# Kernel optimization log

Hardware: AMD Instinct MI355X
Metric: run time of the kernel (lower is better)

## Reference

```python
import jax, jax.numpy as jnp
import numpy as np

BATCH = 1048576
D_IN = 4        # d_in=3 spatial dims + 1 time dim
HID = 64
N_HID_STACK = 4  # hidden residual blocks after the first hidden layer
D_OUT = 3
BN_EPS = 1e-5


def _bn(x, gamma, beta):
    # BatchNorm1d in training mode: biased batch statistics over the batch axis
    mu = jnp.mean(x, axis=0)
    var = jnp.var(x, axis=0)
    return gamma * (x - mu) * jax.lax.rsqrt(var + BN_EPS) + beta


def setup_inputs() -> dict:
    key = jax.random.key(0)
    ks = jax.random.split(key, 8)
    s_in = 1.0 / np.sqrt(D_IN)
    s_h = 1.0 / np.sqrt(HID)
    return {
        "x": jax.random.normal(ks[0], (BATCH, D_IN), dtype=jnp.float32),
        "bn0_gamma": jnp.ones((D_IN,), jnp.float32),
        "bn0_beta": jnp.zeros((D_IN,), jnp.float32),
        "W0": jax.random.normal(ks[1], (D_IN, HID), jnp.float32) * s_in,
        "b0": jnp.zeros((HID,), jnp.float32),
        "gamma0": jnp.ones((HID,), jnp.float32),
        "beta0": jnp.zeros((HID,), jnp.float32),
        "W_hid": jax.random.normal(ks[2], (N_HID_STACK, HID, HID), jnp.float32) * s_h,
        "b_hid": jnp.zeros((N_HID_STACK, HID), jnp.float32),
        "gamma_hid": jnp.ones((N_HID_STACK, HID), jnp.float32),
        "beta_hid": jnp.zeros((N_HID_STACK, HID), jnp.float32),
        "Wout": jax.random.normal(ks[3], (HID, D_OUT), jnp.float32) * s_h,
        "bout": jnp.zeros((D_OUT,), jnp.float32),
    }


def reference(x, bn0_gamma, bn0_beta, W0, b0, gamma0, beta0,
              W_hid, b_hid, gamma_hid, beta_hid, Wout, bout):
    # Net.forward (u-network, single patch, batch_normalization=True, tanh):
    #   x = bn0(x)
    #   y = bn(act(Linear0(x)))                 (first hidden layer, no skip)
    #   y = bn_i(act(Linear_i(y))) + y          (residual hidden layers)
    #   y = Linear_out(y)
    h = _bn(x, bn0_gamma, bn0_beta)
    y = _bn(jnp.tanh(h @ W0 + b0), gamma0, beta0)

    def step(y, layer):
        W, b, g, be = layer
        return _bn(jnp.tanh(y @ W + b), g, be) + y, None

    y, _ = jax.lax.scan(step, y, (W_hid, b_hid, gamma_hid, beta_hid))
    return y @ Wout + bout
```

## Files before the change

kernel.cpp:

```cpp
#include <hip/hip_runtime.h>
#include <stdint.h>


#define NROWS 1048576
#define EPS 1e-5f
#define INV_B 9.5367431640625e-07f
#define LOG2E2 2.885390081777927f
#define BIGGRID 8192

typedef __attribute__((ext_vector_type(8))) short bfrag;
typedef __attribute__((ext_vector_type(4))) float facc;
typedef __attribute__((ext_vector_type(4))) float f4v;

__device__ __forceinline__ float bf2f(short s) {
  union { unsigned u; float f; } v;
  v.u = ((unsigned)(unsigned short)s) << 16;
  return v.f;
}
__device__ __forceinline__ short f2bf(float f) {
  union { float f; unsigned u; } v;
  v.f = f;
  unsigned r = v.u + 0x7FFFu + ((v.u >> 16) & 1u);
  return (short)(r >> 16);
}
__device__ __forceinline__ float tanh_fast(float x) {
  float e = __builtin_amdgcn_exp2f(x * LOG2E2);
  return 1.f - 2.f * __builtin_amdgcn_rcpf(e + 1.f);
}

__device__ __forceinline__ bfrag make_ident(int l15, int q, int p) {
  bfrag r;
  const short one = (short)0x3F80;
#pragma unroll
  for (int j = 0; j < 8; ++j) r[j] = (q * 8 + j == l15 + 16 * p) ? one : 0;
  return r;
}

template <int W>
__global__ __launch_bounds__(256) void k_reduce(const float* __restrict__ P,
                                                float* __restrict__ S,
                                                int rows_per_blk) {
  __shared__ float red[256];
  const int tid = threadIdx.x;
  const int col = tid % W;
  const int grp = tid / W;
  const int G = 256 / W;
  size_t r0 = (size_t)blockIdx.x * rows_per_blk;
  float s = 0.f;
  for (int r = grp; r < rows_per_blk; r += G) s += P[(r0 + r) * W + col];
  red[tid] = s;
  __syncthreads();
  if (tid < W) {
    float t = 0.f;
#pragma unroll 4
    for (int g = 0; g < G; ++g) t += red[g * W + tid];
    atomicAdd(&S[tid], t);
  }
}


__global__ __launch_bounds__(256) void k_stats_x(const float* __restrict__ x,
                                                 float* __restrict__ P) {
  __shared__ float red[4][8];
  const int tid = threadIdx.x;
  const int wave = tid >> 6;
  size_t base = (size_t)blockIdx.x * 1024 + tid;
  float s[4] = {0.f, 0.f, 0.f, 0.f}, q[4] = {0.f, 0.f, 0.f, 0.f};
#pragma unroll
  for (int it = 0; it < 4; ++it) {
    f4v v = *(const f4v*)(x + (base + (size_t)it * 256) * 4);
#pragma unroll
    for (int k = 0; k < 4; ++k) { s[k] += v[k]; q[k] = fmaf(v[k], v[k], q[k]); }
  }
#pragma unroll
  for (int off = 32; off > 0; off >>= 1) {
#pragma unroll
    for (int k = 0; k < 4; ++k) {
      s[k] += __shfl_xor(s[k], off);
      q[k] += __shfl_xor(q[k], off);
    }
  }
  if ((tid & 63) == 0) {
#pragma unroll
    for (int k = 0; k < 4; ++k) { red[wave][k] = s[k]; red[wave][4 + k] = q[k]; }
  }
  __syncthreads();
  if (tid < 8)
    P[blockIdx.x * 8 + tid] =
        red[0][tid] + red[1][tid] + red[2][tid] + red[3][tid];
}

__global__ __launch_bounds__(256) void k_stats_z1(
    const float* __restrict__ x, const float* __restrict__ bn0g,
    const float* __restrict__ bn0b, const float* __restrict__ W0,
    const float* __restrict__ b0, const float* __restrict__ sx,
    float* __restrict__ P) {
  __shared__ float red[2][4][64];
  const int tid = threadIdx.x;
  const int lane = tid & 63;
  const int wave = tid >> 6;
  int gw = blockIdx.x * 4 + wave;
  float sc[4], sh[4];
#pragma unroll
  for (int k = 0; k < 4; ++k) {
    float mean = sx[k] * INV_B;
    float var = fmaf(-mean, mean, sx[4 + k] * INV_B);
    float rs = rsqrtf(var + EPS);
    sc[k] = bn0g[k] * rs;
    sh[k] = fmaf(-sc[k], mean, bn0b[k]);
  }
  float w[4];
#pragma unroll
  for (int k = 0; k < 4; ++k) w[k] = W0[k * 64 + lane];
  float bj = b0[lane];
  float s = 0.f, q = 0.f;
  size_t r0 = (size_t)gw * 256;
  for (int r = 0; r < 256; ++r) {
    f4v xv = *(const f4v*)(x + (r0 + r) * 4);
    float acc = bj;
#pragma unroll
    for (int k = 0; k < 4; ++k)
      acc = fmaf(fmaf(xv[k], sc[k], sh[k]), w[k], acc);
    float z = tanh_fast(acc);
    s += z;
    q = fmaf(z, z, q);
  }
  red[0][wave][lane] = s;
  red[1][wave][lane] = q;
  __syncthreads();
  if (tid < 128) {
    int which = tid >> 6, c = tid & 63;
    P[blockIdx.x * 128 + tid] = red[which][0][c] + red[which][1][c] +
                                red[which][2][c] + red[which][3][c];
  }
}

__global__ __launch_bounds__(256) void k_prep(const float* __restrict__ Wh,
                                              short* __restrict__ WT) {
  int idx = blockIdx.x * 256 + threadIdx.x;
  int l = idx >> 12, rem = idx & 4095, k = rem >> 6, c = rem & 63;
  WT[l * 4096 + c * 64 + k] = f2bf(Wh[l * 4096 + k * 64 + c]);
}


__global__ __launch_bounds__(256) void k_first(
    const float* __restrict__ x, const float* __restrict__ bn0g,
    const float* __restrict__ bn0b, const float* __restrict__ W0,
    const float* __restrict__ b0, const float* __restrict__ gamma0,
    const float* __restrict__ beta0, const float* __restrict__ sx,
    const float* __restrict__ s1, const short* __restrict__ WTb,
    const float* __restrict__ bb, float* __restrict__ P,
    short* __restrict__ Y) {
  __shared__ __align__(16) float lds_x[128 * 4];
  __shared__ __align__(16) short ly[128 * 72];
  __shared__ float lds_st[4][128];

  const int tid = threadIdx.x;
  const int lane = tid & 63;
  const int wave = tid >> 6;
  const int l15 = lane & 15;
  const int q = lane >> 4;
  const int wr = wave * 32;
  const size_t r0 = (size_t)blockIdx.x * 128;

  f4v xp;
  if (lane < 32) xp = *(const f4v*)(x + (r0 + wr + lane) * 4);

  float sc0[4], sh0[4];
#pragma unroll
  for (int k = 0; k < 4; ++k) {
    float mean = sx[k] * INV_B;
    float var = fmaf(-mean, mean, sx[4 + k] * INV_B);
    float rs = rsqrtf(var + EPS);
    sc0[k] = bn0g[k] * rs;
    sh0[k] = fmaf(-sc0[k], mean, bn0b[k]);
  }
  float w0c[4];
#pragma unroll
  for (int k = 0; k < 4; ++k) w0c[k] = W0[k * 64 + lane];
  float b0c = b0[lane];
  float mean1 = s1[lane] * INV_B;
  float var1 = fmaf(-mean1, mean1, s1[64 + lane] * INV_B);
  float A1c = gamma0[lane] * rsqrtf(var1 + EPS);
  float B1c = fmaf(-A1c, mean1, beta0[lane]);

  if (lane < 32) *(f4v*)&lds_x[(wr + lane) * 4] = xp;

  for (int e = 0; e < 32; ++e) {
    int row = wr + e;
    float acc = b0c;
#pragma unroll
    for (int k = 0; k < 4; ++k)
      acc = fmaf(fmaf(lds_x[row * 4 + k], sc0[k], sh0[k]), w0c[k], acc);
    float z = tanh_fast(acc);
    ly[row * 72 + lane] = f2bf(fmaf(A1c, z, B1c));
  }

  bfrag af[2][2];
#pragma unroll
  for (int mt = 0; mt < 2; ++mt)
#pragma unroll
    for (int kt = 0; kt < 2; ++kt) {
      af[mt][kt] =
          *(const bfrag*)&ly[(wr + mt * 16 + l15) * 72 + kt * 32 + q * 8];
      *(bfrag*)(Y + (r0 + wr + mt * 16 + l15) * 64 + kt * 32 + q * 8) =
          af[mt][kt];
    }
  float bbv[4];
  bfrag bwb[4][2];
#pragma unroll
  for (int nt = 0; nt < 4; ++nt) {
    bbv[nt] = bb[nt * 16 + l15];
#pragma unroll
    for (int kt = 0; kt < 2; ++kt)
      bwb[nt][kt] =
          *(const bfrag*)(WTb + (nt * 16 + l15) * 64 + kt * 32 + q * 8);
  }
  facc acc2[2][4];
#pragma unroll
  for (int mt = 0; mt < 2; ++mt)
#pragma unroll
    for (int nt = 0; nt < 4; ++nt) {
      acc2[mt][nt][0] = bbv[nt]; acc2[mt][nt][1] = bbv[nt];
      acc2[mt][nt][2] = bbv[nt]; acc2[mt][nt][3] = bbv[nt];
    }
#pragma unroll
  for (int mt = 0; mt < 2; ++mt)
#pragma unroll
    for (int nt = 0; nt < 4; ++nt)
#pragma unroll
      for (int kt = 0; kt < 2; ++kt)
        acc2[mt][nt] = __builtin_amdgcn_mfma_f32_16x16x32_bf16(
            af[mt][kt], bwb[nt][kt], acc2[mt][nt], 0, 0, 0);
#pragma unroll
  for (int nt = 0; nt < 4; ++nt) {
    float s = 0.f, ss = 0.f;
#pragma unroll
    for (int mt = 0; mt < 2; ++mt)
#pragma unroll
      for (int i = 0; i < 4; ++i) {
        float z = tanh_fast(acc2[mt][nt][i]);
        s += z;
        ss = fmaf(z, z, ss);
      }
    s += __shfl_xor(s, 16); s += __shfl_xor(s, 32);
    ss += __shfl_xor(ss, 16); ss += __shfl_xor(ss, 32);
    if (q == 0) {
      lds_st[wave][nt * 16 + l15] = s;
      lds_st[wave][64 + nt * 16 + l15] = ss;
    }
  }
  __syncthreads();
  if (tid < 128)
    P[(size_t)blockIdx.x * 128 + tid] =
        lds_st[0][tid] + lds_st[1][tid] + lds_st[2][tid] + lds_st[3][tid];
}

__global__ __launch_bounds__(256) void k_mid(
    short* __restrict__ Y, const short* __restrict__ WTa,
    const float* __restrict__ ba, const float* __restrict__ ga,
    const float* __restrict__ bea, const float* __restrict__ sa,
    const short* __restrict__ WTb, const float* __restrict__ bb,
    float* __restrict__ P, int rev) {
  __shared__ __align__(16) short ly[128 * 72];
  __shared__ float lds_st[4][128];

  const int tid = threadIdx.x;
  const int lane = tid & 63;
  const int wave = tid >> 6;
  const int l15 = lane & 15;
  const int q = lane >> 4;
  const int wr = wave * 32;
  const int bid = rev ? ((int)gridDim.x - 1 - (int)blockIdx.x) : (int)blockIdx.x;
  const size_t r0 = (size_t)bid * 128;

  bfrag af[2][2];
#pragma unroll
  for (int mt = 0; mt < 2; ++mt)
#pragma unroll
    for (int kt = 0; kt < 2; ++kt)
      af[mt][kt] =
          *(const bfrag*)(Y + (r0 + wr + mt * 16 + l15) * 64 + kt * 32 + q * 8);

  float Av[4], Bv[4], bav[4];
#pragma unroll
  for (int nt = 0; nt < 4; ++nt) {
    int c = nt * 16 + l15;
    float mean = sa[c] * INV_B;
    float var = fmaf(-mean, mean, sa[64 + c] * INV_B);
    float A = ga[c] * rsqrtf(var + EPS);
    Av[nt] = A;
    Bv[nt] = fmaf(-A, mean, bea[c]);
    bav[nt] = ba[c];
  }
  bfrag bwa[4][2];
#pragma unroll
  for (int nt = 0; nt < 4; ++nt)
#pragma unroll
    for (int kt = 0; kt < 2; ++kt)
      bwa[nt][kt] =
          *(const bfrag*)(WTa + (nt * 16 + l15) * 64 + kt * 32 + q * 8);
  const bfrag bI0 = make_ident(l15, q, 0);
  const bfrag bI1 = make_ident(l15, q, 1);

#pragma unroll
  for (int mt = 0; mt < 2; ++mt) {
    facc acc[4], yC[4];
#pragma unroll
    for (int nt = 0; nt < 4; ++nt) {
      acc[nt][0] = bav[nt]; acc[nt][1] = bav[nt];
      acc[nt][2] = bav[nt]; acc[nt][3] = bav[nt];
      yC[nt][0] = 0.f; yC[nt][1] = 0.f; yC[nt][2] = 0.f; yC[nt][3] = 0.f;
    }
#pragma unroll
    for (int nt = 0; nt < 4; ++nt) {
#pragma unroll
      for (int kt = 0; kt < 2; ++kt)
        acc[nt] = __builtin_amdgcn_mfma_f32_16x16x32_bf16(
            af[mt][kt], bwa[nt][kt], acc[nt], 0, 0, 0);
      yC[nt] = __builtin_amdgcn_mfma_f32_16x16x32_bf16(
          af[mt][nt >> 1], (nt & 1) ? bI1 : bI0, yC[nt], 0, 0, 0);
    }
#pragma unroll
    for (int nt = 0; nt < 4; ++nt) {
      int c = nt * 16 + l15;
      float A = Av[nt], Bc = Bv[nt];
#pragma unroll
      for (int i = 0; i < 4; ++i) {
        int rl = wr + mt * 16 + q * 4 + i;
        float z = tanh_fast(acc[nt][i]);
        ly[rl * 72 + c] = f2bf(fmaf(A, z, Bc) + yC[nt][i]);
      }
    }
  }

#pragma unroll
  for (int mt = 0; mt < 2; ++mt)
#pragma unroll
    for (int kt = 0; kt < 2; ++kt) {
      af[mt][kt] =
          *(const bfrag*)&ly[(wr + mt * 16 + l15) * 72 + kt * 32 + q * 8];
      *(bfrag*)(Y + (r0 + wr + mt * 16 + l15) * 64 + kt * 32 + q * 8) =
          af[mt][kt];
    }
  float bbv[4];
  bfrag bwb[4][2];
#pragma unroll
  for (int nt = 0; nt < 4; ++nt) {
    bbv[nt] = bb[nt * 16 + l15];
#pragma unroll
    for (int kt = 0; kt < 2; ++kt)
      bwb[nt][kt] =
          *(const bfrag*)(WTb + (nt * 16 + l15) * 64 + kt * 32 + q * 8);
  }
  facc acc2[2][4];
#pragma unroll
  for (int mt = 0; mt < 2; ++mt)
#pragma unroll
    for (int nt = 0; nt < 4; ++nt) {
      acc2[mt][nt][0] = bbv[nt]; acc2[mt][nt][1] = bbv[nt];
      acc2[mt][nt][2] = bbv[nt]; acc2[mt][nt][3] = bbv[nt];
    }
#pragma unroll
  for (int mt = 0; mt < 2; ++mt)
#pragma unroll
    for (int nt = 0; nt < 4; ++nt)
#pragma unroll
      for (int kt = 0; kt < 2; ++kt)
        acc2[mt][nt] = __builtin_amdgcn_mfma_f32_16x16x32_bf16(
            af[mt][kt], bwb[nt][kt], acc2[mt][nt], 0, 0, 0);
#pragma unroll
  for (int nt = 0; nt < 4; ++nt) {
    float s = 0.f, ss = 0.f;
#pragma unroll
    for (int mt = 0; mt < 2; ++mt)
#pragma unroll
      for (int i = 0; i < 4; ++i) {
        float z = tanh_fast(acc2[mt][nt][i]);
        s += z;
        ss = fmaf(z, z, ss);
      }
    s += __shfl_xor(s, 16); s += __shfl_xor(s, 32);
    ss += __shfl_xor(ss, 16); ss += __shfl_xor(ss, 32);
    if (q == 0) {
      lds_st[wave][nt * 16 + l15] = s;
      lds_st[wave][64 + nt * 16 + l15] = ss;
    }
  }
  __syncthreads();
  if (tid < 128)
    P[(size_t)bid * 128 + tid] =
        lds_st[0][tid] + lds_st[1][tid] + lds_st[2][tid] + lds_st[3][tid];
}

__global__ __launch_bounds__(256) void k_last(
    const short* __restrict__ Y, const short* __restrict__ WTa,
    const float* __restrict__ ba, const float* __restrict__ ga,
    const float* __restrict__ bea, const float* __restrict__ sa,
    const float* __restrict__ Wout, const float* __restrict__ bout,
    float* __restrict__ out) {
  const int tid = threadIdx.x;
  const int lane = tid & 63;
  const int wave = tid >> 6;
  const int l15 = lane & 15;
  const int q = lane >> 4;
  const int wr = wave * 32;
  const size_t r0 = (size_t)blockIdx.x * 128;

  bfrag af[2][2];
#pragma unroll
  for (int mt = 0; mt < 2; ++mt)
#pragma unroll
    for (int kt = 0; kt < 2; ++kt)
      af[mt][kt] =
          *(const bfrag*)(Y + (r0 + wr + mt * 16 + l15) * 64 + kt * 32 + q * 8);

  float Av[4], Bv[4], bav[4], wo[4][3];
#pragma unroll
  for (int nt = 0; nt < 4; ++nt) {
    int c = nt * 16 + l15;
    float mean = sa[c] * INV_B;
    float var = fmaf(-mean, mean, sa[64 + c] * INV_B);
    float A = ga[c] * rsqrtf(var + EPS);
    Av[nt] = A;
    Bv[nt] = fmaf(-A, mean, bea[c]);
    bav[nt] = ba[c];
#pragma unroll
    for (int o = 0; o < 3; ++o) wo[nt][o] = Wout[c * 3 + o];
  }
  bfrag bwa[4][2];
#pragma unroll
  for (int nt = 0; nt < 4; ++nt)
#pragma unroll
    for (int kt = 0; kt < 2; ++kt)
      bwa[nt][kt] =
          *(const bfrag*)(WTa + (nt * 16 + l15) * 64 + kt * 32 + q * 8);
  const bfrag bI0 = make_ident(l15, q, 0);
  const bfrag bI1 = make_ident(l15, q, 1);
  float bo0 = bout[0], bo1 = bout[1], bo2 = bout[2];

#pragma unroll
  for (int mt = 0; mt < 2; ++mt) {
    facc acc[4], yC[4];
#pragma unroll
    for (int nt = 0; nt < 4; ++nt) {
      acc[nt][0] = bav[nt]; acc[nt][1] = bav[nt];
      acc[nt][2] = bav[nt]; acc[nt][3] = bav[nt];
      yC[nt][0] = 0.f; yC[nt][1] = 0.f; yC[nt][2] = 0.f; yC[nt][3] = 0.f;
    }
#pragma unroll
    for (int nt = 0; nt < 4; ++nt) {
#pragma unroll
      for (int kt = 0; kt < 2; ++kt)
        acc[nt] = __builtin_amdgcn_mfma_f32_16x16x32_bf16(
            af[mt][kt], bwa[nt][kt], acc[nt], 0, 0, 0);
      yC[nt] = __builtin_amdgcn_mfma_f32_16x16x32_bf16(
          af[mt][nt >> 1], (nt & 1) ? bI1 : bI0, yC[nt], 0, 0, 0);
    }
#pragma unroll
    for (int i = 0; i < 4; ++i) {
      float o0 = 0.f, o1 = 0.f, o2 = 0.f;
#pragma unroll
      for (int nt = 0; nt < 4; ++nt) {
        float z = tanh_fast(acc[nt][i]);
        float yn = bf2f(f2bf(fmaf(Av[nt], z, Bv[nt]) + yC[nt][i]));
        o0 = fmaf(yn, wo[nt][0], o0);
        o1 = fmaf(yn, wo[nt][1], o1);
        o2 = fmaf(yn, wo[nt][2], o2);
      }
#pragma unroll
      for (int off = 1; off < 16; off <<= 1) {
        o0 += __shfl_xor(o0, off);
        o1 += __shfl_xor(o1, off);
        o2 += __shfl_xor(o2, off);
      }
      if (l15 == 0) {
        size_t ro = (r0 + wr + mt * 16 + q * 4 + i) * 3;
        out[ro] = o0 + bo0;
        out[ro + 1] = o1 + bo1;
        out[ro + 2] = o2 + bo2;
      }
    }
  }
}

extern "C" void kernel_launch(void* const* d_in, const int* in_sizes, int n_in,
                              void* d_out, int out_size, void* d_ws,
                              size_t ws_size, hipStream_t stream) {
  (void)in_sizes; (void)n_in; (void)out_size; (void)ws_size;
  const float* x = (const float*)d_in[0];
  const float* bn0g = (const float*)d_in[1];
  const float* bn0b = (const float*)d_in[2];
  const float* W0 = (const float*)d_in[3];
  const float* b0 = (const float*)d_in[4];
  const float* gamma0 = (const float*)d_in[5];
  const float* beta0 = (const float*)d_in[6];
  const float* Wh = (const float*)d_in[7];
  const float* bh = (const float*)d_in[8];
  const float* gh = (const float*)d_in[9];
  const float* beh = (const float*)d_in[10];
  const float* Wout = (const float*)d_in[11];
  const float* bout = (const float*)d_in[12];
  float* out = (float*)d_out;

  char* ws = (char*)d_ws;
  short* Y = (short*)ws;
  const size_t YB = (size_t)NROWS * 64 * 2;
  float* stats = (float*)(ws + YB);
  float* Sx = stats;
  float* S1 = stats + 8;
  float* S2 = stats + 136;
  float* S3 = stats + 264;
  float* S4 = stats + 392;
  float* S5 = stats + 520;
  short* WT = (short*)(ws + YB + 4096);
  float* P = (float*)(ws + YB + 4096 + 32768);

  hipMemsetAsync(stats, 0, 648 * sizeof(float), stream);
  k_prep<<<64, 256, 0, stream>>>(Wh, WT);
  k_stats_x<<<1024, 256, 0, stream>>>(x, P);
  k_reduce<8><<<8, 256, 0, stream>>>(P, Sx, 128);
  k_stats_z1<<<1024, 256, 0, stream>>>(x, bn0g, bn0b, W0, b0, Sx, P);
  k_reduce<128><<<8, 256, 0, stream>>>(P, S1, 128);
  k_first<<<BIGGRID, 256, 0, stream>>>(x, bn0g, bn0b, W0, b0, gamma0, beta0,
                                       Sx, S1, WT, bh, P, Y);
  k_reduce<128><<<64, 256, 0, stream>>>(P, S2, 128);
  k_mid<<<BIGGRID, 256, 0, stream>>>(Y, WT, bh, gh, beh, S2, WT + 4096,
                                     bh + 64, P, 1);
  k_reduce<128><<<64, 256, 0, stream>>>(P, S3, 128);
  k_mid<<<BIGGRID, 256, 0, stream>>>(Y, WT + 4096, bh + 64, gh + 64, beh + 64,
                                     S3, WT + 2 * 4096, bh + 128, P, 0);
  k_reduce<128><<<64, 256, 0, stream>>>(P, S4, 128);
  k_mid<<<BIGGRID, 256, 0, stream>>>(Y, WT + 2 * 4096, bh + 128, gh + 128,
                                     beh + 128, S4, WT + 3 * 4096, bh + 192, P,
                                     1);
  k_reduce<128><<<64, 256, 0, stream>>>(P, S5, 128);
  k_last<<<BIGGRID, 256, 0, stream>>>(Y, WT + 3 * 4096, bh + 192, gh + 192,
                                      beh + 192, S5, Wout, bout, out);
}
```

Baseline: 603.5 us.

## Fuse whole network into one persistent cooperative kernel with grid syncs

Replaces the chain of per-layer kernels and reduce kernels with a single persistent cooperative kernel. Blocks loop over row tiles and exchange BatchNorm statistics through grid.sync-based two-level reductions. This removes roughly a dozen kernel launches and their tail and drain gaps. In exchange it caps occupancy at about two blocks per CU, adds grid-wide barriers, and drops the alternating tile order that used to reuse cache between layers. The old multi-kernel path is kept as a fallback if the cooperative launch fails.

New measurement: 900.1 us. 49.1% more time.

```diff
diff --git a/kernel.cpp b/kernel.cpp
--- a/kernel.cpp
+++ b/kernel.cpp
@@ -1,12 +1,15 @@
 #include <hip/hip_runtime.h>
+#include <hip/hip_cooperative_groups.h>
 #include <stdint.h>
 
+namespace cg = cooperative_groups;
+
 
 #define NROWS 1048576
+#define NTILES 8192
 #define EPS 1e-5f
 #define INV_B 9.5367431640625e-07f
 #define LOG2E2 2.885390081777927f
-#define BIGGRID 8192
 
 typedef __attribute__((ext_vector_type(8))) short bfrag;
 typedef __attribute__((ext_vector_type(4))) float facc;
@@ -27,7 +30,6 @@
   float e = __builtin_amdgcn_exp2f(x * LOG2E2);
   return 1.f - 2.f * __builtin_amdgcn_rcpf(e + 1.f);
 }
-
 __device__ __forceinline__ bfrag make_ident(int l15, int q, int p) {
   bfrag r;
   const short one = (short)0x3F80;
@@ -35,6 +37,433 @@
   for (int j = 0; j < 8; ++j) r[j] = (q * 8 + j == l15 + 16 * p) ? one : 0;
   return r;
 }
+
+
+__device__ __forceinline__ void grid_reduce128(float* __restrict__ P,
+                                               float* __restrict__ P2,
+                                               float* S_lds, float* red_l,
+                                               int bid, int tid, int nblk,
+                                               cg::grid_group& grid) {
+  grid.sync();
+  if (bid < 128 && tid < 128) {
+    float s = 0.f;
+    for (int r = bid; r < nblk; r += 128) s += P[(size_t)r * 128 + tid];
+    P2[bid * 128 + tid] = s;
+  }
+  grid.sync();
+  {
+    int col = tid & 127, g = tid >> 7;
+    float s = 0.f;
+    for (int r = g * 64; r < g * 64 + 64; ++r) s += P2[r * 128 + col];
+    red_l[tid] = s;
+    __syncthreads();
+    if (tid < 128) S_lds[tid] = red_l[tid] + red_l[128 + tid];
+    __syncthreads();
+  }
+}
+
+__global__ __launch_bounds__(256, 2) void k_net(
+    const float* __restrict__ x, const float* __restrict__ bn0g,
+    const float* __restrict__ bn0b, const float* __restrict__ W0,
+    const float* __restrict__ b0, const float* __restrict__ gamma0,
+    const float* __restrict__ beta0, const float* __restrict__ Wh,
+    const float* __restrict__ bh, const float* __restrict__ gh,
+    const float* __restrict__ beh, const float* __restrict__ Wout,
+    const float* __restrict__ bout, short* __restrict__ WT,
+    float* __restrict__ P, float* __restrict__ P2, short* __restrict__ Y,
+    float* __restrict__ out) {
+  cg::grid_group grid = cg::this_grid();
+
+  __shared__ __align__(16) short ly[128 * 72];
+  __shared__ __align__(16) float lds_x[128 * 4];
+  __shared__ float lds_st[4][128];
+  __shared__ float S_lds[128];
+  __shared__ float red_l[256];
+
+  const int tid = threadIdx.x;
+  const int lane = tid & 63;
+  const int wave = tid >> 6;
+  const int l15 = lane & 15;
+  const int q = lane >> 4;
+  const int wr = wave * 32;
+  const int bid = blockIdx.x;
+  const int nblk = (int)gridDim.x;
+
+  for (int i = bid * 256 + tid; i < 16384; i += nblk * 256) {
+    int l = i >> 12, rem = i & 4095, k = rem >> 6, c = rem & 63;
+    WT[l * 4096 + c * 64 + k] = f2bf(Wh[l * 4096 + k * 64 + c]);
+  }
+  {
+    float s[4] = {0.f, 0.f, 0.f, 0.f}, qq[4] = {0.f, 0.f, 0.f, 0.f};
+    for (int c = bid; c < 1024; c += nblk) {
+      size_t base = (size_t)c * 1024 + tid;
+#pragma unroll
+      for (int it = 0; it < 4; ++it) {
+        f4v v = *(const f4v*)(x + (base + (size_t)it * 256) * 4);
+#pragma unroll
+        for (int k = 0; k < 4; ++k) {
+          s[k] += v[k];
+          qq[k] = fmaf(v[k], v[k], qq[k]);
+        }
+      }
+    }
+#pragma unroll
+    for (int off = 32; off > 0; off >>= 1) {
+#pragma unroll
+      for (int k = 0; k < 4; ++k) {
+        s[k] += __shfl_xor(s[k], off);
+        qq[k] += __shfl_xor(qq[k], off);
+      }
+    }
+    if (lane == 0) {
+#pragma unroll
+      for (int k = 0; k < 4; ++k) {
+        lds_st[wave][k] = s[k];
+        lds_st[wave][4 + k] = qq[k];
+      }
+    }
+    __syncthreads();
+    if (tid < 8)
+      P[(size_t)bid * 128 + tid] = lds_st[0][tid] + lds_st[1][tid] +
+                                   lds_st[2][tid] + lds_st[3][tid];
+  }
+  grid.sync();
+  {
+    int col = tid & 7, grp = tid >> 3;
+    float s = 0.f;
+    for (int r = grp; r < nblk; r += 32) s += P[(size_t)r * 128 + col];
+    red_l[tid] = s;
+    __syncthreads();
+    if (tid < 8) {
+      float t = 0.f;
+#pragma unroll
+      for (int g = 0; g < 32; ++g) t += red_l[g * 8 + tid];
+      S_lds[tid] = t;
+    }
+    __syncthreads();
+  }
+  float sc0[4], sh0[4];
+#pragma unroll
+  for (int k = 0; k < 4; ++k) {
+    float mean = S_lds[k] * INV_B;
+    float var = fmaf(-mean, mean, S_lds[4 + k] * INV_B);
+    float rs = rsqrtf(var + EPS);
+    sc0[k] = bn0g[k] * rs;
+    sh0[k] = fmaf(-sc0[k], mean, bn0b[k]);
+  }
+  float w0c[4];
+#pragma unroll
+  for (int k = 0; k < 4; ++k) w0c[k] = W0[k * 64 + lane];
+  float b0c = b0[lane];
+
+  {
+    float s = 0.f, qq = 0.f;
+    for (int c = bid; c < 1024; c += nblk) {
+      size_t r0 = (size_t)c * 1024 + (size_t)wave * 256;
+      for (int r = 0; r < 256; ++r) {
+        f4v xv = *(const f4v*)(x + (r0 + r) * 4);
+        float acc = b0c;
+#pragma unroll
+        for (int k = 0; k < 4; ++k)
+          acc = fmaf(fmaf(xv[k], sc0[k], sh0[k]), w0c[k], acc);
+        float z = tanh_fast(acc);
+        s += z;
+        qq = fmaf(z, z, qq);
+      }
+    }
+    __syncthreads();
+    lds_st[wave][lane] = s;
+    lds_st[wave][64 + lane] = qq;
+    __syncthreads();
+    if (tid < 128)
+      P[(size_t)bid * 128 + tid] = lds_st[0][tid] + lds_st[1][tid] +
+                                   lds_st[2][tid] + lds_st[3][tid];
+  }
+  grid_reduce128(P, P2, S_lds, red_l, bid, tid, nblk, grid);
+  float mean1 = S_lds[lane] * INV_B;
+  float var1 = fmaf(-mean1, mean1, S_lds[64 + lane] * INV_B);
+  float A1c = gamma0[lane] * rsqrtf(var1 + EPS);
+  float B1c = fmaf(-A1c, mean1, beta0[lane]);
+
+  {
+    float bbv[4];
+    bfrag bwb[4][2];
+#pragma unroll
+    for (int nt = 0; nt < 4; ++nt) {
+      bbv[nt] = bh[nt * 16 + l15];
+#pragma unroll
+      for (int kt = 0; kt < 2; ++kt)
+        bwb[nt][kt] =
+            *(const bfrag*)(WT + (nt * 16 + l15) * 64 + kt * 32 + q * 8);
+    }
+    float sAcc[4] = {0.f, 0.f, 0.f, 0.f}, qAcc[4] = {0.f, 0.f, 0.f, 0.f};
+    for (int t = bid; t < NTILES; t += nblk) {
+      const size_t r0 = (size_t)t * 128;
+      if (lane < 32)
+        *(f4v*)&lds_x[(wr + lane) * 4] =
+            *(const f4v*)(x + (r0 + wr + lane) * 4);
+      for (int e = 0; e < 32; ++e) {
+        int row = wr + e;
+        float acc = b0c;
+#pragma unroll
+        for (int k = 0; k < 4; ++k)
+          acc = fmaf(fmaf(lds_x[row * 4 + k], sc0[k], sh0[k]), w0c[k], acc);
+        float z = tanh_fast(acc);
+        ly[row * 72 + lane] = f2bf(fmaf(A1c, z, B1c));
+      }
+      bfrag af[2][2];
+#pragma unroll
+      for (int mt = 0; mt < 2; ++mt)
+#pragma unroll
+        for (int kt = 0; kt < 2; ++kt) {
+          af[mt][kt] =
+              *(const bfrag*)&ly[(wr + mt * 16 + l15) * 72 + kt * 32 + q * 8];
+          *(bfrag*)(Y + (r0 + wr + mt * 16 + l15) * 64 + kt * 32 + q * 8) =
+              af[mt][kt];
+        }
+      facc acc2[2][4];
+#pragma unroll
+      for (int mt = 0; mt < 2; ++mt)
+#pragma unroll
+        for (int nt = 0; nt < 4; ++nt) {
+          acc2[mt][nt][0] = bbv[nt]; acc2[mt][nt][1] = bbv[nt];
+          acc2[mt][nt][2] = bbv[nt]; acc2[mt][nt][3] = bbv[nt];
+        }
+#pragma unroll
+      for (int mt = 0; mt < 2; ++mt)
+#pragma unroll
+        for (int nt = 0; nt < 4; ++nt)
+#pragma unroll
+          for (int kt = 0; kt < 2; ++kt)
+            acc2[mt][nt] = __builtin_amdgcn_mfma_f32_16x16x32_bf16(
+                af[mt][kt], bwb[nt][kt], acc2[mt][nt], 0, 0, 0);
+#pragma unroll
+      for (int nt = 0; nt < 4; ++nt)
+#pragma unroll
+        for (int mt = 0; mt < 2; ++mt)
+#pragma unroll
+          for (int i = 0; i < 4; ++i) {
+            float z = tanh_fast(acc2[mt][nt][i]);
+            sAcc[nt] += z;
+            qAcc[nt] = fmaf(z, z, qAcc[nt]);
+          }
+    }
+    __syncthreads();
+#pragma unroll
+    for (int nt = 0; nt < 4; ++nt) {
+      float s = sAcc[nt], ss = qAcc[nt];
+      s += __shfl_xor(s, 16); s += __shfl_xor(s, 32);
+      ss += __shfl_xor(ss, 16); ss += __shfl_xor(ss, 32);
+      if (q == 0) {
+        lds_st[wave][nt * 16 + l15] = s;
+        lds_st[wave][64 + nt * 16 + l15] = ss;
+      }
+    }
+    __syncthreads();
+    if (tid < 128)
+      P[(size_t)bid * 128 + tid] = lds_st[0][tid] + lds_st[1][tid] +
+                                   lds_st[2][tid] + lds_st[3][tid];
+  }
+  grid_reduce128(P, P2, S_lds, red_l, bid, tid, nblk, grid);
+
+  const bfrag bI0 = make_ident(l15, q, 0);
+  const bfrag bI1 = make_ident(l15, q, 1);
+  for (int layer = 0; layer < 3; ++layer) {
+    float Av[4], Bv[4], bav[4], bbv[4];
+#pragma unroll
+    for (int nt = 0; nt < 4; ++nt) {
+      int c = nt * 16 + l15;
+      float mean = S_lds[c] * INV_B;
+      float var = fmaf(-mean, mean, S_lds[64 + c] * INV_B);
+      float A = gh[layer * 64 + c] * rsqrtf(var + EPS);
+      Av[nt] = A;
+      Bv[nt] = fmaf(-A, mean, beh[layer * 64 + c]);
+      bav[nt] = bh[layer * 64 + c];
+      bbv[nt] = bh[(layer + 1) * 64 + c];
+    }
+    bfrag bwa[4][2], bwb[4][2];
+#pragma unroll
+    for (int nt = 0; nt < 4; ++nt)
+#pragma unroll
+      for (int kt = 0; kt < 2; ++kt) {
+        bwa[nt][kt] = *(const bfrag*)(WT + layer * 4096 +
+                                      (nt * 16 + l15) * 64 + kt * 32 + q * 8);
+        bwb[nt][kt] = *(const bfrag*)(WT + (layer + 1) * 4096 +
+                                      (nt * 16 + l15) * 64 + kt * 32 + q * 8);
+      }
+    float sAcc[4] = {0.f, 0.f, 0.f, 0.f}, qAcc[4] = {0.f, 0.f, 0.f, 0.f};
+    for (int t = bid; t < NTILES; t += nblk) {
+      const size_t r0 = (size_t)t * 128;
+      bfrag af[2][2];
+#pragma unroll
+      for (int mt = 0; mt < 2; ++mt)
+#pragma unroll
+        for (int kt = 0; kt < 2; ++kt)
+          af[mt][kt] = *(const bfrag*)(Y + (r0 + wr + mt * 16 + l15) * 64 +
+                                       kt * 32 + q * 8);
+#pragma unroll
+      for (int mt = 0; mt < 2; ++mt) {
+        facc acc[4], yC[4];
+#pragma unroll
+        for (int nt = 0; nt < 4; ++nt) {
+          acc[nt][0] = bav[nt]; acc[nt][1] = bav[nt];
+          acc[nt][2] = bav[nt]; acc[nt][3] = bav[nt];
+          yC[nt][0] = 0.f; yC[nt][1] = 0.f; yC[nt][2] = 0.f; yC[nt][3] = 0.f;
+        }
+#pragma unroll
+        for (int nt = 0; nt < 4; ++nt) {
+#pragma unroll
+          for (int kt = 0; kt < 2; ++kt)
+            acc[nt] = __builtin_amdgcn_mfma_f32_16x16x32_bf16(
+                af[mt][kt], bwa[nt][kt], acc[nt], 0, 0, 0);
+          yC[nt] = __builtin_amdgcn_mfma_f32_16x16x32_bf16(
+              af[mt][nt >> 1], (nt & 1) ? bI1 : bI0, yC[nt], 0, 0, 0);
+        }
+#pragma unroll
+        for (int nt = 0; nt < 4; ++nt) {
+          int c = nt * 16 + l15;
+          float A = Av[nt], Bc = Bv[nt];
+#pragma unroll
+          for (int i = 0; i < 4; ++i) {
+            int rl = wr + mt * 16 + q * 4 + i;
+            float z = tanh_fast(acc[nt][i]);
+            ly[rl * 72 + c] = f2bf(fmaf(A, z, Bc) + yC[nt][i]);
+          }
+        }
+      }
+      bfrag af2[2][2];
+#pragma unroll
+      for (int mt = 0; mt < 2; ++mt)
+#pragma unroll
+        for (int kt = 0; kt < 2; ++kt) {
+          af2[mt][kt] =
+              *(const bfrag*)&ly[(wr + mt * 16 + l15) * 72 + kt * 32 + q * 8];
+          *(bfrag*)(Y + (r0 + wr + mt * 16 + l15) * 64 + kt * 32 + q * 8) =
+              af2[mt][kt];
+        }
+      facc acc2[2][4];
+#pragma unroll
+      for (int mt = 0; mt < 2; ++mt)
+#pragma unroll
+        for (int nt = 0; nt < 4; ++nt) {
+          acc2[mt][nt][0] = bbv[nt]; acc2[mt][nt][1] = bbv[nt];
+          acc2[mt][nt][2] = bbv[nt]; acc2[mt][nt][3] = bbv[nt];
+        }
+#pragma unroll
+      for (int mt = 0; mt < 2; ++mt)
+#pragma unroll
+        for (int nt = 0; nt < 4; ++nt)
+#pragma unroll
+          for (int kt = 0; kt < 2; ++kt)
+            acc2[mt][nt] = __builtin_amdgcn_mfma_f32_16x16x32_bf16(
+                af2[mt][kt], bwb[nt][kt], acc2[mt][nt], 0, 0, 0);
+#pragma unroll
+      for (int nt = 0; nt < 4; ++nt)
+#pragma unroll
+        for (int mt = 0; mt < 2; ++mt)
+#pragma unroll
+          for (int i = 0; i < 4; ++i) {
+            float z = tanh_fast(acc2[mt][nt][i]);
+            sAcc[nt] += z;
+            qAcc[nt] = fmaf(z, z, qAcc[nt]);
+          }
+    }
+    __syncthreads();
+#pragma unroll
+    for (int nt = 0; nt < 4; ++nt) {
+      float s = sAcc[nt], ss = qAcc[nt];
+      s += __shfl_xor(s, 16); s += __shfl_xor(s, 32);
+      ss += __shfl_xor(ss, 16); ss += __shfl_xor(ss, 32);
+      if (q == 0) {
+        lds_st[wave][nt * 16 + l15] = s;
+        lds_st[wave][64 + nt * 16 + l15] = ss;
+      }
+    }
+    __syncthreads();
+    if (tid < 128)
+      P[(size_t)bid * 128 + tid] = lds_st[0][tid] + lds_st[1][tid] +
+                                   lds_st[2][tid] + lds_st[3][tid];
+    grid_reduce128(P, P2, S_lds, red_l, bid, tid, nblk, grid);
+  }
+
+  {
+    float Av[4], Bv[4], bav[4], wo[4][3];
+#pragma unroll
+    for (int nt = 0; nt < 4; ++nt) {
+      int c = nt * 16 + l15;
+      float mean = S_lds[c] * INV_B;
+      float var = fmaf(-mean, mean, S_lds[64 + c] * INV_B);
+      float A = gh[3 * 64 + c] * rsqrtf(var + EPS);
+      Av[nt] = A;
+      Bv[nt] = fmaf(-A, mean, beh[3 * 64 + c]);
+      bav[nt] = bh[3 * 64 + c];
+#pragma unroll
+      for (int o = 0; o < 3; ++o) wo[nt][o] = Wout[c * 3 + o];
+    }
+    bfrag bwa[4][2];
+#pragma unroll
+    for (int nt = 0; nt < 4; ++nt)
+#pragma unroll
+      for (int kt = 0; kt < 2; ++kt)
+        bwa[nt][kt] = *(const bfrag*)(WT + 3 * 4096 + (nt * 16 + l15) * 64 +
+                                      kt * 32 + q * 8);
+    float bo0 = bout[0], bo1 = bout[1], bo2 = bout[2];
+    for (int t = bid; t < NTILES; t += nblk) {
+      const size_t r0 = (size_t)t * 128;
+      bfrag af[2][2];
+#pragma unroll
+      for (int mt = 0; mt < 2; ++mt)
+#pragma unroll
+        for (int kt = 0; kt < 2; ++kt)
+          af[mt][kt] = *(const bfrag*)(Y + (r0 + wr + mt * 16 + l15) * 64 +
+                                       kt * 32 + q * 8);
+#pragma unroll
+      for (int mt = 0; mt < 2; ++mt) {
+        facc acc[4], yC[4];
+#pragma unroll
+        for (int nt = 0; nt < 4; ++nt) {
+          acc[nt][0] = bav[nt]; acc[nt][1] = bav[nt];
+          acc[nt][2] = bav[nt]; acc[nt][3] = bav[nt];
+          yC[nt][0] = 0.f; yC[nt][1] = 0.f; yC[nt][2] = 0.f; yC[nt][3] = 0.f;
+        }
+#pragma unroll
+        for (int nt = 0; nt < 4; ++nt) {
+#pragma unroll
+          for (int kt = 0; kt < 2; ++kt)
+            acc[nt] = __builtin_amdgcn_mfma_f32_16x16x32_bf16(
+                af[mt][kt], bwa[nt][kt], acc[nt], 0, 0, 0);
+          yC[nt] = __builtin_amdgcn_mfma_f32_16x16x32_bf16(
+              af[mt][nt >> 1], (nt & 1) ? bI1 : bI0, yC[nt], 0, 0, 0);
+        }
+#pragma unroll
+        for (int i = 0; i < 4; ++i) {
+          float o0 = 0.f, o1 = 0.f, o2 = 0.f;
+#pragma unroll
+          for (int nt = 0; nt < 4; ++nt) {
+            float z = tanh_fast(acc[nt][i]);
+            float yn = bf2f(f2bf(fmaf(Av[nt], z, Bv[nt]) + yC[nt][i]));
+            o0 = fmaf(yn, wo[nt][0], o0);
+            o1 = fmaf(yn, wo[nt][1], o1);
+            o2 = fmaf(yn, wo[nt][2], o2);
+          }
+#pragma unroll
+          for (int off = 1; off < 16; off <<= 1) {
+            o0 += __shfl_xor(o0, off);
+            o1 += __shfl_xor(o1, off);
+            o2 += __shfl_xor(o2, off);
+          }
+          if (l15 == 0) {
+            size_t ro = (r0 + wr + mt * 16 + q * 4 + i) * 3;
+            out[ro] = o0 + bo0;
+            out[ro + 1] = o1 + bo1;
+            out[ro + 2] = o2 + bo2;
+          }
+        }
+      }
+    }
+  }
+}
+
 
 template <int W>
 __global__ __launch_bounds__(256) void k_reduce(const float* __restrict__ P,
@@ -58,7 +487,6 @@
   }
 }
 
-
 __global__ __launch_bounds__(256) void k_stats_x(const float* __restrict__ x,
                                                  float* __restrict__ P) {
   __shared__ float red[4][8];
@@ -142,7 +570,6 @@
   WT[l * 4096 + c * 64 + k] = f2bf(Wh[l * 4096 + k * 64 + c]);
 }
 
-
 __global__ __launch_bounds__(256) void k_first(
     const float* __restrict__ x, const float* __restrict__ bn0g,
     const float* __restrict__ bn0b, const float* __restrict__ W0,
@@ -261,7 +688,7 @@
     const float* __restrict__ ba, const float* __restrict__ ga,
     const float* __restrict__ bea, const float* __restrict__ sa,
     const short* __restrict__ WTb, const float* __restrict__ bb,
-    float* __restrict__ P, int rev) {
+    float* __restrict__ P) {
   __shared__ __align__(16) short ly[128 * 72];
   __shared__ float lds_st[4][128];
 
@@ -271,8 +698,7 @@
   const int l15 = lane & 15;
   const int q = lane >> 4;
   const int wr = wave * 32;
-  const int bid = rev ? ((int)gridDim.x - 1 - (int)blockIdx.x) : (int)blockIdx.x;
-  const size_t r0 = (size_t)bid * 128;
+  const size_t r0 = (size_t)blockIdx.x * 128;
 
   bfrag af[2][2];
 #pragma unroll
@@ -389,7 +815,7 @@
   }
   __syncthreads();
   if (tid < 128)
-    P[(size_t)bid * 128 + tid] =
+    P[(size_t)blockIdx.x * 128 + tid] =
         lds_st[0][tid] + lds_st[1][tid] + lds_st[2][tid] + lds_st[3][tid];
 }
 
@@ -506,35 +932,57 @@
   char* ws = (char*)d_ws;
   short* Y = (short*)ws;
   const size_t YB = (size_t)NROWS * 64 * 2;
-  float* stats = (float*)(ws + YB);
+  short* WT = (short*)(ws + YB);
+  float* P = (float*)(ws + YB + 32768);
+  float* P2 = (float*)(ws + YB + 32768 + 524288);
+  float* stats = (float*)(ws + YB + 32768 + 524288 + 65536);
+  float* Pmk = (float*)(ws + YB + 32768 + 524288 + 65536 + 4096);
+
+  int maxb = 0;
+  hipError_t oe =
+      hipOccupancyMaxActiveBlocksPerMultiprocessor(&maxb, k_net, 256, 0);
+  int nblk = (oe == hipSuccess) ? maxb * 256 : 0;
+  if (nblk > 1024) nblk = 1024;
+  nblk = (nblk / 128) * 128;
+
+  hipError_t le = hipErrorUnknown;
+  if (nblk >= 128) {
+    void* args[] = {(void*)&x,      (void*)&bn0g, (void*)&bn0b, (void*)&W0,
+                    (void*)&b0,     (void*)&gamma0, (void*)&beta0,
+                    (void*)&Wh,     (void*)&bh,   (void*)&gh,   (void*)&beh,
+                    (void*)&Wout,   (void*)&bout, (void*)&WT,   (void*)&P,
+                    (void*)&P2,     (void*)&Y,    (void*)&out};
+    le = hipLaunchCooperativeKernel((const void*)k_net, dim3(nblk), dim3(256),
+                                    args, 0, stream);
+  }
+  if (le == hipSuccess) return;
+  (void)hipGetLastError();
+
   float* Sx = stats;
   float* S1 = stats + 8;
   float* S2 = stats + 136;
   float* S3 = stats + 264;
   float* S4 = stats + 392;
   float* S5 = stats + 520;
-  short* WT = (short*)(ws + YB + 4096);
-  float* P = (float*)(ws + YB + 4096 + 32768);
 
   hipMemsetAsync(stats, 0, 648 * sizeof(float), stream);
   k_prep<<<64, 256, 0, stream>>>(Wh, WT);
-  k_stats_x<<<1024, 256, 0, stream>>>(x, P);
-  k_reduce<8><<<8, 256, 0, stream>>>(P, Sx, 128);
-  k_stats_z1<<<1024, 256, 0, stream>>>(x, bn0g, bn0b, W0, b0, Sx, P);
-  k_reduce<128><<<8, 256, 0, stream>>>(P, S1, 128);
-  k_first<<<BIGGRID, 256, 0, stream>>>(x, bn0g, bn0b, W0, b0, gamma0, beta0,
-                                       Sx, S1, WT, bh, P, Y);
-  k_reduce<128><<<64, 256, 0, stream>>>(P, S2, 128);
-  k_mid<<<BIGGRID, 256, 0, stream>>>(Y, WT, bh, gh, beh, S2, WT + 4096,
-                                     bh + 64, P, 1);
-  k_reduce<128><<<64, 256, 0, stream>>>(P, S3, 128);
-  k_mid<<<BIGGRID, 256, 0, stream>>>(Y, WT + 4096, bh + 64, gh + 64, beh + 64,
-                                     S3, WT + 2 * 4096, bh + 128, P, 0);
-  k_reduce<128><<<64, 256, 0, stream>>>(P, S4, 128);
-  k_mid<<<BIGGRID, 256, 0, stream>>>(Y, WT + 2 * 4096, bh + 128, gh + 128,
-                                     beh + 128, S4, WT + 3 * 4096, bh + 192, P,
-                                     1);
-  k_reduce<128><<<64, 256, 0, stream>>>(P, S5, 128);
-  k_last<<<BIGGRID, 256, 0, stream>>>(Y, WT + 3 * 4096, bh + 192, gh + 192,
-                                      beh + 192, S5, Wout, bout, out);
-}
+  k_stats_x<<<1024, 256, 0, stream>>>(x, Pmk);
+  k_reduce<8><<<8, 256, 0, stream>>>(Pmk, Sx, 128);
+  k_stats_z1<<<1024, 256, 0, stream>>>(x, bn0g, bn0b, W0, b0, Sx, Pmk);
+  k_reduce<128><<<8, 256, 0, stream>>>(Pmk, S1, 128);
+  k_first<<<8192, 256, 0, stream>>>(x, bn0g, bn0b, W0, b0, gamma0, beta0, Sx,
+                                    S1, WT, bh, Pmk, Y);
+  k_reduce<128><<<64, 256, 0, stream>>>(Pmk, S2, 128);
+  k_mid<<<8192, 256, 0, stream>>>(Y, WT, bh, gh, beh, S2, WT + 4096, bh + 64,
+                                  Pmk);
+  k_reduce<128><<<64, 256, 0, stream>>>(Pmk, S3, 128);
+  k_mid<<<8192, 256, 0, stream>>>(Y, WT + 4096, bh + 64, gh + 64, beh + 64, S3,
+                                  WT + 2 * 4096, bh + 128, Pmk);
+  k_reduce<128><<<64, 256, 0, stream>>>(Pmk, S4, 128);
+  k_mid<<<8192, 256, 0, stream>>>(Y, WT + 2 * 4096, bh + 128, gh + 128,
+                                  beh + 128, S4, WT + 3 * 4096, bh + 192, Pmk);
+  k_reduce<128><<<64, 256, 0, stream>>>(Pmk, S5, 128);
+  k_last<<<8192, 256, 0, stream>>>(Y, WT + 3 * 4096, bh + 192, gh + 192,
+                                   beh + 192, S5, Wout, bout, out);
+}
```
